# Kernel optimization log

Measured on AMD Instinct MI355X. Metric: run time of the kernel, lower is better.

Reference implementation:

```python
import jax, jax.numpy as jnp
import numpy as np

NUM_HEADS = 16

def setup_inputs() -> dict:
    key = jax.random.key(0)
    k1, k2, k3, k4 = jax.random.split(key, 4)
    B, S, D = 4, 4096, 2048
    scale = 1.0 / np.sqrt(D)
    return {
        "x": jax.random.normal(k1, (B, S, D), dtype=jnp.float32),
        "W_q": jax.random.normal(k2, (D, D), dtype=jnp.float32) * scale,
        "W_kv": jax.random.normal(k3, (D, D), dtype=jnp.float32) * scale,
        "W_o": jax.random.normal(k4, (D, D), dtype=jnp.float32) * scale,
    }

def _l2_normalize_complex(z):
    # torch.norm(z, dim=-1, keepdim=True) for complex: sqrt(sum |z|^2)
    n = jnp.sqrt(jnp.sum(jnp.abs(z) ** 2, axis=-1, keepdims=True))
    return z / n

def reference(x, W_q, W_kv, W_o):
    B, S, D = x.shape
    H = NUM_HEADS
    hd = D // H
    # Linear (no bias), torch convention: x @ W.T
    q = (x @ W_q.T).reshape(B, S, H, hd)
    kv = (x @ W_kv.T).reshape(B, S, H, hd)
    # HRR binding: FFT along head dim
    qf = jnp.fft.fft(q, axis=-1)
    kvf = jnp.fft.fft(kv, axis=-1)
    qf = _l2_normalize_complex(qf)
    kvf = _l2_normalize_complex(kvf)
    # causal=True: cumulative sum of bound key-values over sequence
    kvf = jnp.cumsum(kvf, axis=1)
    qv = qf * kvf
    values_hat = jnp.fft.ifft(qv, axis=-1).real.astype(x.dtype)
    values_hat = values_hat.reshape(B, S, D)
    return values_hat @ W_o.T
```

## Files before the change

### kernel.cpp

```cpp
#include <hip/hip_runtime.h>
#include <hip/hip_bf16.h>


typedef unsigned short u16;
typedef unsigned int u32;
typedef __attribute__((ext_vector_type(8))) short short8;
typedef __attribute__((ext_vector_type(4))) float f32x4;

__device__ __forceinline__ float bf2f(u16 u) {
  u32 x = ((u32)u) << 16;
  float f; __builtin_memcpy(&f, &x, 4); return f;
}
__device__ __forceinline__ u16 f2bf(float f) {
  __hip_bfloat16 h = __float2bfloat16(f);
  u16 u; __builtin_memcpy(&u, &h, 2); return u;
}
__device__ __forceinline__ u32 pack2(float a, float b) {
  return (u32)f2bf(a) | ((u32)f2bf(b) << 16);
}

#define GLD16(gp, lp)                                                        \
  __builtin_amdgcn_global_load_lds(                                          \
      (const __attribute__((address_space(1))) void*)(gp),                   \
      (__attribute__((address_space(3))) void*)(lp), 16, 0, 0)

template <int EPI, bool FOLD>
__global__ __launch_bounds__(256, 2) void gemm_bt(
    const u16* __restrict__ A, const u16* __restrict__ B, void* __restrict__ C,
    int M, int N, int K, int lda) {
  const int ntiles = N >> 7;
  const int bid = blockIdx.x;
  const int bm = bid / ntiles, bn = bid % ntiles;
  const long rowBase = (long)bm * 128, colBase = (long)bn * 128;
  const long aOff = FOLD ? colBase : 0;
  const long bRowBase = FOLD ? 0 : colBase;

  __shared__ u16 As[128 * 32];
  __shared__ u16 Bs[128 * 32];
  __shared__ float ssbuf[128][2];

  const int tid = threadIdx.x;
  const int wave = tid >> 6, lane = tid & 63;
  const int quad = lane >> 4, l16 = lane & 15;
  const int waveRow = (wave >> 1) * 64, waveCol = (wave & 1) * 64;

  const int srow = lane >> 2, scol = (lane & 3) * 8;
  const u16* pa = A + (rowBase + wave * 32 + srow) * (long)lda + aOff + scol;
  const u16* pb = B + (bRowBase + wave * 32 + srow) * (long)K + scol;
  u16* lA0 = &As[(wave * 32) * 32];
  u16* lA1 = &As[(wave * 32 + 16) * 32];
  u16* lB0 = &Bs[(wave * 32) * 32];
  u16* lB1 = &Bs[(wave * 32 + 16) * 32];

  f32x4 acc[4][4] = {};

  for (int kt = 0; kt < K; kt += 32) {
    GLD16(pa + kt, lA0);
    GLD16(pa + kt + 16 * (long)lda, lA1);
    GLD16(pb + kt, lB0);
    GLD16(pb + kt + 16 * (long)K, lB1);
    __syncthreads();

    short8 af[4], bfr[4];
#pragma unroll
    for (int i = 0; i < 4; i++)
      af[i] = *(const short8*)&As[(waveRow + i * 16 + l16) * 32 + quad * 8];
#pragma unroll
    for (int j = 0; j < 4; j++)
      bfr[j] = *(const short8*)&Bs[(waveCol + j * 16 + l16) * 32 + quad * 8];
#pragma unroll
    for (int i = 0; i < 4; i++)
#pragma unroll
      for (int j = 0; j < 4; j++)
        acc[i][j] = __builtin_amdgcn_mfma_f32_16x16x32_bf16(af[i], bfr[j], acc[i][j], 0, 0, 0);
    __syncthreads();
  }

  float scl[4][4];
#pragma unroll
  for (int i = 0; i < 4; i++)
#pragma unroll
    for (int r = 0; r < 4; r++) scl[i][r] = 1.0f;

  if (EPI == 2) {
#pragma unroll
    for (int i = 0; i < 4; i++) {
#pragma unroll
      for (int r = 0; r < 4; r++) {
        float s = 0.f;
#pragma unroll
        for (int j = 0; j < 4; j++) { float v = acc[i][j][r]; s += v * v; }
#pragma unroll
        for (int m = 1; m < 16; m <<= 1) s += __shfl_xor(s, m);
        if (l16 == 0) ssbuf[waveRow + i * 16 + quad * 4 + r][wave & 1] = s;
      }
    }
    __syncthreads();
#pragma unroll
    for (int i = 0; i < 4; i++)
#pragma unroll
      for (int r = 0; r < 4; r++) {
        int row = waveRow + i * 16 + quad * 4 + r;
        scl[i][r] = rsqrtf(128.0f * (ssbuf[row][0] + ssbuf[row][1]));
      }
  }

#pragma unroll
  for (int i = 0; i < 4; i++) {
#pragma unroll
    for (int j = 0; j < 4; j++) {
      long row0 = rowBase + waveRow + i * 16 + quad * 4;
      long col = colBase + waveCol + j * 16 + l16;
#pragma unroll
      for (int r = 0; r < 4; r++) {
        float v = acc[i][j][r] * scl[i][r];
        long off = (row0 + r) * (long)N + col;
        if (EPI == 0) ((float*)C)[off] = v;
        else          ((u16*)C)[off] = f2bf(v);
      }
    }
  }
}

__global__ __launch_bounds__(256) void cast_f2b(const float* __restrict__ in,
                                                u16* __restrict__ out, int n4) {
  int i = blockIdx.x * 256 + threadIdx.x;
  if (i >= n4) return;
  float4 v = ((const float4*)in)[i];
  ushort4 u;
  u.x = f2bf(v.x); u.y = f2bf(v.y); u.z = f2bf(v.z); u.w = f2bf(v.w);
  ((ushort4*)out)[i] = u;
}

__global__ __launch_bounds__(256) void init_mats(u16* __restrict__ CSp,
                                                 u16* __restrict__ W2pT) {
  int idx = blockIdx.x * 256 + threadIdx.x;
  const float PI64 = 3.14159265358979323846f / 64.0f;
  if (idx < 16384) {
    int p = idx >> 7, n = idx & 127;
    int k = p >> 1;
    float v;
    if (p == 1) v = (n & 1) ? -1.f : 1.f;
    else {
      int t = (k * n) & 127;
      float ang = (float)t * PI64;
      v = (p & 1) ? -sinf(ang) : cosf(ang);
    }
    CSp[p * 128 + n] = f2bf(v);
  } else {
    int r = idx - 16384;
    int p = r >> 7, d = r & 127;
    int k = p >> 1;
    float v;
    if (p == 0) v = 1.0f / 128.0f;
    else if (p == 1) v = ((d & 1) ? -1.f : 1.f) / 128.0f;
    else {
      int t = (k * d) & 127;
      float ang = (float)t * PI64;
      v = ((p & 1) ? -2.f * sinf(ang) : 2.f * cosf(ang)) / 128.0f;
    }
    W2pT[p * 128 + d] = f2bf(v);
  }
}

__global__ __launch_bounds__(64) void scan_chunksum(const u16* __restrict__ F,
                                                    float* __restrict__ part) {
  int blk = blockIdx.x;
  int c = blk & 63, bh = blk >> 6;
  int h = bh & 15, b = bh >> 4;
  int l = threadIdx.x;
  float s0 = 0.f, s1 = 0.f;
  for (int t = c * 64; t < c * 64 + 64; ++t) {
    u32 u = ((const u32*)(F + ((long)(b * 4096 + t) * 32 + 16 + h) * 128))[l];
    s0 += bf2f((u16)(u & 0xffff));
    s1 += bf2f((u16)(u >> 16));
  }
  float2 w; w.x = s0; w.y = s1;
  ((float2*)part)[(long)blk * 64 + l] = w;
}

__global__ __launch_bounds__(128) void scan_exclusive(float* __restrict__ part) {
  int bh = blockIdx.x;
  int j = threadIdx.x;
  float run = 0.f;
  for (int c = 0; c < 64; ++c) {
    long idx = ((long)(bh * 64 + c)) * 128 + j;
    float v = part[idx];
    part[idx] = run;
    run += v;
  }
}

__global__ __launch_bounds__(64) void scan_main(const u16* __restrict__ F,
                                                u16* __restrict__ QV,
                                                const float* __restrict__ part) {
  int blk = blockIdx.x;
  int c = blk & 63, bh = blk >> 6;
  int h = bh & 15, b = bh >> 4;
  int l = threadIdx.x;
  float2 cc = ((const float2*)part)[(long)blk * 64 + l];
  float cr = cc.x, ci = cc.y;
  for (int t = c * 64; t < c * 64 + 64; ++t) {
    long m = (long)(b * 4096 + t);
    u32 ku = ((const u32*)(F + (m * 32 + 16 + h) * 128))[l];
    u32 qu = ((const u32*)(F + (m * 32 + h) * 128))[l];
    float kr = bf2f((u16)(ku & 0xffff)), ki = bf2f((u16)(ku >> 16));
    float qr = bf2f((u16)(qu & 0xffff)), qi = bf2f((u16)(qu >> 16));
    cr += kr; ci += ki;
    float vr, vi;
    if (l == 0) { vr = qr * cr; vi = qi * ci; }
    else { vr = qr * cr - qi * ci; vi = qr * ci + qi * cr; }
    ((u32*)(QV + (m * 16 + h) * 128))[l] = pack2(vr, vi);
  }
}

extern "C" void kernel_launch(void* const* d_in, const int* in_sizes, int n_in,
                              void* d_out, int out_size, void* d_ws, size_t ws_size,
                              hipStream_t stream) {
  const float* x   = (const float*)d_in[0];
  const float* Wq  = (const float*)d_in[1];
  const float* Wkv = (const float*)d_in[2];
  const float* Wo  = (const float*)d_in[3];
  float* out = (float*)d_out;

  const long M1 = 16384;
  const long D = 2048;
  const long R = M1 * 16;
  const long XE = M1 * D;
  const long WE = D * D;

  char* ws = (char*)d_ws;
  u16* qkh  = (u16*)(ws);
  u16* F    = (u16*)(ws + 134217728);
  u16* xb   = (u16*)(ws + 268435456);
  u16* wqkb = (u16*)(ws + 335544320);
  u16* wob  = (u16*)(ws + 352321536);
  u16* wo2  = (u16*)(ws + 360710144);
  u16* CSp  = (u16*)(ws + 369098752);
  u16* W2pT = (u16*)(ws + 369131520);
  float* part = (float*)(ws + 369164288);
  u16* QV = qkh;

  cast_f2b<<<(int)(XE / 4 / 256), 256, 0, stream>>>(x, xb, (int)(XE / 4));
  cast_f2b<<<(int)(WE / 4 / 256), 256, 0, stream>>>(Wq, wqkb, (int)(WE / 4));
  cast_f2b<<<(int)(WE / 4 / 256), 256, 0, stream>>>(Wkv, wqkb + WE, (int)(WE / 4));
  cast_f2b<<<(int)(WE / 4 / 256), 256, 0, stream>>>(Wo, wob, (int)(WE / 4));
  init_mats<<<128, 256, 0, stream>>>(CSp, W2pT);

  gemm_bt<1, true><<<16 * 16, 256, 0, stream>>>(wob, W2pT, wo2, 2048, 2048, 128, 2048);

  gemm_bt<2, false><<<(int)((M1 / 128) * (4096 / 128)), 256, 0, stream>>>(
      xb, wqkb, qkh, (int)M1, 4096, (int)D, (int)D);

  gemm_bt<1, false><<<(int)(2 * R / 128), 256, 0, stream>>>(
      qkh, CSp, F, (int)(2 * R), 128, 128, 128);

  scan_chunksum<<<64 * 64, 64, 0, stream>>>(F, part);
  scan_exclusive<<<64, 128, 0, stream>>>(part);
  scan_main<<<64 * 64, 64, 0, stream>>>(F, QV, part);

  gemm_bt<0, false><<<(int)((M1 / 128) * (D / 128)), 256, 0, stream>>>(
      QV, wo2, out, (int)M1, (int)D, (int)D, (int)D);
}
```

Measured before the change: 831.3 us.

## Add 256x256-tile 512-thread pipelined GEMM for the two large projections

Introduces a new GEMM kernel with 256x256 output tiles, 8 waves, a BK=64 double-buffered LDS pipeline using direct global-to-LDS loads, XOR-swizzled LDS reads, phased MFMA/load interleaving with setprio, and workgroup remapping across groups of 8. The fused QK projection and the output projection switch to it. The goal is higher arithmetic intensity and better overlap of loads with MFMA in the dominant GEMMs. It uses 128KB of LDS per workgroup and many accumulator registers, which limits occupancy. The EPI==2 row-norm epilogue is reimplemented for the larger tile.

```diff
diff --git a/kernel.cpp b/kernel.cpp
--- a/kernel.cpp
+++ b/kernel.cpp
@@ -23,6 +23,220 @@
   __builtin_amdgcn_global_load_lds(                                          \
       (const __attribute__((address_space(1))) void*)(gp),                   \
       (__attribute__((address_space(3))) void*)(lp), 16, 0, 0)
+
+#define BARX()                                                               \
+  do {                                                                       \
+    asm volatile("" ::: "memory");                                           \
+    __builtin_amdgcn_s_barrier();                                            \
+    asm volatile("" ::: "memory");                                           \
+  } while (0)
+
+template <int EPI>
+__global__ __launch_bounds__(512, 2) void gemm256(
+    const u16* __restrict__ A, const u16* __restrict__ B, void* __restrict__ C,
+    int N, int K) {
+  __shared__ alignas(1024) char smem[131072];
+  const int NT = K >> 6;
+  const int ntn = N >> 8;
+  const int nwg = gridDim.x;
+  int wg = blockIdx.x;
+  wg = (wg & 7) * (nwg >> 3) + (wg >> 3);
+  const int bm = wg / ntn, bn = wg % ntn;
+  const long rowBase = (long)bm << 8, colBase = (long)bn << 8;
+
+  const int tid = threadIdx.x;
+  const int w = tid >> 6, lane = tid & 63;
+  const int quad = lane >> 4, l16 = lane & 15;
+  const int wm = w >> 2, wn = w & 3;
+
+  const int grow = w * 8 + (lane >> 3);
+  const int gcol = ((lane & 7) * 8) ^ ((lane >> 4) << 4);
+  const u16* pa[2][2];
+  const u16* pb[2][2];
+#pragma unroll
+  for (int h = 0; h < 2; h++)
+#pragma unroll
+    for (int r = 0; r < 2; r++) {
+      pa[h][r] = A + (rowBase + h * 128 + r * 64 + grow) * (long)K + gcol;
+      pb[h][r] = B + (colBase + h * 128 + r * 64 + grow) * (long)K + gcol;
+    }
+  char* ldsA = smem;
+  char* ldsB = smem + 65536;
+
+#define STG_A(v, h)                                                          \
+  do {                                                                       \
+    char* d_ = ldsA + (((v)&1) << 15) + ((h) << 14) + (w << 10);             \
+    GLD16(pa[h][0] + (long)(v) * 64, d_);                                    \
+    GLD16(pa[h][1] + (long)(v) * 64, d_ + 8192);                             \
+  } while (0)
+#define STG_B(v, h)                                                          \
+  do {                                                                       \
+    char* d_ = ldsB + (((v)&1) << 15) + ((h) << 14) + (w << 10);             \
+    GLD16(pb[h][0] + (long)(v) * 64, d_);                                    \
+    GLD16(pb[h][1] + (long)(v) * 64, d_ + 8192);                             \
+  } while (0)
+
+  const int cb0 = (quad << 4) ^ (((l16 >> 1) & 3) << 5);
+  const int cb1 = cb0 ^ 64;
+  const char* rdA = ldsA + (wm * 128 + l16) * 128;
+  const char* rdB = ldsB + (wn * 64 + l16) * 128;
+
+  short8 a_[8], bl[4], bh[4];
+  f32x4 acc[8][4] = {};
+
+  STG_A(0, 0); STG_A(0, 1); STG_B(0, 0); STG_B(0, 1);
+  STG_B(1, 0); STG_B(1, 1);
+  asm volatile("s_waitcnt vmcnt(4)" ::: "memory");
+  BARX();
+
+#define PH_TOP(U)                                                            \
+  const char* ab = rdA + (((U)&1) << 15);                                    \
+  const char* bb = rdB + (((U)&1) << 15);
+
+#define PH0(U, SA_)                                                          \
+  do {                                                                       \
+    PH_TOP(U)                                                                \
+    _Pragma("unroll") for (int i = 0; i < 4; i++) {                          \
+      a_[2*i]   = *(const short8*)(ab + i * 2048 + cb0);                     \
+      a_[2*i+1] = *(const short8*)(ab + i * 2048 + cb1);                     \
+    }                                                                        \
+    _Pragma("unroll") for (int j = 0; j < 2; j++) {                          \
+      bl[2*j]   = *(const short8*)(bb + j * 2048 + cb0);                     \
+      bl[2*j+1] = *(const short8*)(bb + j * 2048 + cb1);                     \
+    }                                                                        \
+    if (SA_) STG_A((U) + 1, 0);                                              \
+    BARX();                                                                  \
+    __builtin_amdgcn_s_setprio(1);                                           \
+    _Pragma("unroll") for (int i = 0; i < 4; i++)                            \
+      _Pragma("unroll") for (int j = 0; j < 2; j++) {                        \
+        acc[i][j] = __builtin_amdgcn_mfma_f32_16x16x32_bf16(a_[2*i],   bl[2*j],   acc[i][j], 0, 0, 0); \
+        acc[i][j] = __builtin_amdgcn_mfma_f32_16x16x32_bf16(a_[2*i+1], bl[2*j+1], acc[i][j], 0, 0, 0); \
+      }                                                                      \
+    __builtin_amdgcn_s_setprio(0);                                           \
+    BARX();                                                                  \
+  } while (0)
+
+#define PH1(U, SA_)                                                          \
+  do {                                                                       \
+    PH_TOP(U)                                                                \
+    _Pragma("unroll") for (int j = 0; j < 2; j++) {                          \
+      bh[2*j]   = *(const short8*)(bb + (j + 2) * 2048 + cb0);               \
+      bh[2*j+1] = *(const short8*)(bb + (j + 2) * 2048 + cb1);               \
+    }                                                                        \
+    if (SA_) STG_A((U) + 1, 1);                                              \
+    BARX();                                                                  \
+    __builtin_amdgcn_s_setprio(1);                                           \
+    _Pragma("unroll") for (int i = 0; i < 4; i++)                            \
+      _Pragma("unroll") for (int j = 0; j < 2; j++) {                        \
+        acc[i][j+2] = __builtin_amdgcn_mfma_f32_16x16x32_bf16(a_[2*i],   bh[2*j],   acc[i][j+2], 0, 0, 0); \
+        acc[i][j+2] = __builtin_amdgcn_mfma_f32_16x16x32_bf16(a_[2*i+1], bh[2*j+1], acc[i][j+2], 0, 0, 0); \
+      }                                                                      \
+    __builtin_amdgcn_s_setprio(0);                                           \
+    BARX();                                                                  \
+  } while (0)
+
+#define PH2(U, SB_)                                                          \
+  do {                                                                       \
+    PH_TOP(U)                                                                \
+    _Pragma("unroll") for (int i = 0; i < 4; i++) {                          \
+      a_[2*i]   = *(const short8*)(ab + (i + 4) * 2048 + cb0);               \
+      a_[2*i+1] = *(const short8*)(ab + (i + 4) * 2048 + cb1);               \
+    }                                                                        \
+    if (SB_) STG_B((U) + 2, 0);                                              \
+    BARX();                                                                  \
+    __builtin_amdgcn_s_setprio(1);                                           \
+    _Pragma("unroll") for (int i = 0; i < 4; i++)                            \
+      _Pragma("unroll") for (int j = 0; j < 2; j++) {                        \
+        acc[i+4][j] = __builtin_amdgcn_mfma_f32_16x16x32_bf16(a_[2*i],   bl[2*j],   acc[i+4][j], 0, 0, 0); \
+        acc[i+4][j] = __builtin_amdgcn_mfma_f32_16x16x32_bf16(a_[2*i+1], bl[2*j+1], acc[i+4][j], 0, 0, 0); \
+      }                                                                      \
+    __builtin_amdgcn_s_setprio(0);                                           \
+    BARX();                                                                  \
+  } while (0)
+
+#define PH3(U, SB_, WAITSTMT)                                                \
+  do {                                                                       \
+    if (SB_) STG_B((U) + 2, 1);                                              \
+    BARX();                                                                  \
+    __builtin_amdgcn_s_setprio(1);                                           \
+    _Pragma("unroll") for (int i = 0; i < 4; i++)                            \
+      _Pragma("unroll") for (int j = 0; j < 2; j++) {                        \
+        acc[i+4][j+2] = __builtin_amdgcn_mfma_f32_16x16x32_bf16(a_[2*i],   bh[2*j],   acc[i+4][j+2], 0, 0, 0); \
+        acc[i+4][j+2] = __builtin_amdgcn_mfma_f32_16x16x32_bf16(a_[2*i+1], bh[2*j+1], acc[i+4][j+2], 0, 0, 0); \
+      }                                                                      \
+    __builtin_amdgcn_s_setprio(0);                                           \
+    WAITSTMT;                                                                \
+    BARX();                                                                  \
+  } while (0)
+
+  for (int u = 0; u < NT - 2; ++u) {
+    PH0(u, true); PH1(u, true); PH2(u, true);
+    PH3(u, true, asm volatile("s_waitcnt vmcnt(4)" ::: "memory"));
+  }
+  {
+    const int u = NT - 2;
+    PH0(u, true); PH1(u, true); PH2(u, false);
+    PH3(u, false, asm volatile("s_waitcnt vmcnt(0)" ::: "memory"));
+  }
+  {
+    const int u = NT - 1;
+    PH0(u, false); PH1(u, false); PH2(u, false);
+    PH3(u, false, (void)0);
+  }
+#undef PH0
+#undef PH1
+#undef PH2
+#undef PH3
+#undef PH_TOP
+#undef STG_A
+#undef STG_B
+
+  float scl[8][4];
+#pragma unroll
+  for (int i = 0; i < 8; i++)
+#pragma unroll
+    for (int r = 0; r < 4; r++) scl[i][r] = 1.0f;
+
+  if (EPI == 2) {
+    float* ssb = (float*)smem;
+#pragma unroll
+    for (int i = 0; i < 8; i++)
+#pragma unroll
+      for (int r = 0; r < 4; r++) {
+        float s = 0.f;
+#pragma unroll
+        for (int j = 0; j < 4; j++) { float v = acc[i][j][r]; s += v * v; }
+        s += __shfl_xor(s, 1); s += __shfl_xor(s, 2);
+        s += __shfl_xor(s, 4); s += __shfl_xor(s, 8);
+        if (l16 == 0) ssb[((wm * 128 + i * 16 + quad * 4 + r) << 2) + wn] = s;
+      }
+    __syncthreads();
+#pragma unroll
+    for (int i = 0; i < 8; i++)
+#pragma unroll
+      for (int r = 0; r < 4; r++) {
+        int row = wm * 128 + i * 16 + quad * 4 + r;
+        float s = ssb[(row << 2) + (wn & 2)] + ssb[(row << 2) + (wn & 2) + 1];
+        scl[i][r] = rsqrtf(128.0f * s);
+      }
+  }
+
+#pragma unroll
+  for (int i = 0; i < 8; i++) {
+#pragma unroll
+    for (int j = 0; j < 4; j++) {
+      long row0 = rowBase + wm * 128 + i * 16 + quad * 4;
+      long col = colBase + wn * 64 + j * 16 + l16;
+#pragma unroll
+      for (int r = 0; r < 4; r++) {
+        float v = acc[i][j][r] * scl[i][r];
+        long off = (row0 + r) * (long)N + col;
+        if (EPI == 0) ((float*)C)[off] = v;
+        else          ((u16*)C)[off] = f2bf(v);
+      }
+    }
+  }
+}
 
 template <int EPI, bool FOLD>
 __global__ __launch_bounds__(256, 2) void gemm_bt(
@@ -249,8 +463,8 @@
 
   gemm_bt<1, true><<<16 * 16, 256, 0, stream>>>(wob, W2pT, wo2, 2048, 2048, 128, 2048);
 
-  gemm_bt<2, false><<<(int)((M1 / 128) * (4096 / 128)), 256, 0, stream>>>(
-      xb, wqkb, qkh, (int)M1, 4096, (int)D, (int)D);
+  gemm256<2><<<(int)((M1 / 256) * (4096 / 256)), 512, 0, stream>>>(
+      xb, wqkb, qkh, 4096, (int)D);
 
   gemm_bt<1, false><<<(int)(2 * R / 128), 256, 0, stream>>>(
       qkh, CSp, F, (int)(2 * R), 128, 128, 128);
@@ -259,6 +473,6 @@
   scan_exclusive<<<64, 128, 0, stream>>>(part);
   scan_main<<<64 * 64, 64, 0, stream>>>(F, QV, part);
 
-  gemm_bt<0, false><<<(int)((M1 / 128) * (D / 128)), 256, 0, stream>>>(
-      QV, wo2, out, (int)M1, (int)D, (int)D, (int)D);
-}
+  gemm256<0><<<(int)((M1 / 256) * (D / 256)), 512, 0, stream>>>(
+      QV, wo2, out, (int)D, (int)D);
+}
```

Measured after the change: 739.4 us. 1.12x faster.
